# Kernel optimization log

Hardware: AMD Instinct MI355X
Metric: run time of the kernel (lower is better)

## Reference

```python
import jax, jax.numpy as jnp
import numpy as np

TEMPERATURE = 0.1

def setup_inputs() -> dict:
    key = jax.random.key(0)
    ks = jax.random.split(key, 6)
    B, K, D, H, N = 256, 32, 128, 256, 16
    z = jax.random.normal(ks[0], (B, K, D), dtype=jnp.float32)
    # edge MLP params: Linear(2D->H), GELU, Linear(H->D)
    W1 = jax.random.normal(ks[1], (2 * D, H), dtype=jnp.float32) * (1.0 / np.sqrt(2 * D))
    b1 = jnp.zeros((H,), dtype=jnp.float32)
    W2 = jax.random.normal(ks[2], (H, D), dtype=jnp.float32) * (1.0 / np.sqrt(H))
    b2 = jnp.zeros((D,), dtype=jnp.float32)
    codebook = jax.random.normal(ks[3], (N, D), dtype=jnp.float32) * 0.02
    return {"z": z, "W1": W1, "b1": b1, "W2": W2, "b2": b2, "codebook": codebook}

def reference(z, W1, b1, W2, b2, codebook):
    # z: (B,K,D). Edge MLP on concat([z_i, z_j]) == split-weight GEMMs,
    # avoiding materializing the (B,K,K,2D) concat tensor.
    D = z.shape[-1]
    h_i = jnp.einsum('bkd,dh->bkh', z, W1[:D])   # contribution of z_i
    h_j = jnp.einsum('bkd,dh->bkh', z, W1[D:])   # contribution of z_j
    h = h_i[:, :, None, :] + h_j[:, None, :, :] + b1       # (B,K,K,H)
    h = jax.nn.gelu(h, approximate=False)                    # torch nn.GELU default = exact erf
    e_ij = jnp.einsum('bijh,hd->bijd', h, W2) + b2           # (B,K,K,D)
    logits = jnp.einsum('bijd,nd->bijn', e_ij, codebook) / TEMPERATURE  # (B,K,K,N)
    alpha_ij = jax.nn.softmax(logits, axis=-1)
    m_ij = jnp.einsum('bijn,nd->bijd', alpha_ij, codebook)   # (B,K,K,D)
    return (m_ij, alpha_ij, e_ij, logits)
```

## Files before the change

kernel.cpp:

```cpp
#include <hip/hip_runtime.h>
#include <hip/hip_bf16.h>
#include <math.h>

#define BB 256
#define KK 32
#define DD 128
#define HH 256
#define NN 16
#define O0 ((size_t)0)
#define O1 ((size_t)33554432)
#define O2 ((size_t)37748736)
#define O3 ((size_t)71303168)

typedef float f32x4 __attribute__((ext_vector_type(4)));
typedef short s16x8 __attribute__((ext_vector_type(8)));

static __device__ __forceinline__ short f2bf(float x) {
  __hip_bfloat16 h = __float2bfloat16(x);
  return *reinterpret_cast<short*>(&h);
}
static __device__ __forceinline__ float bf2f(short s) {
  __hip_bfloat16 h;
  *reinterpret_cast<short*>(&h) = s;
  return __bfloat162float(h);
}

__global__ __launch_bounds__(256) void hproj_kernel(
    const float* __restrict__ z, const float* __restrict__ W1,
    float* __restrict__ Hi, float* __restrict__ Hj) {
  __shared__ float sz[16][128];
  const int tid = threadIdx.x;
  const int row0 = blockIdx.x * 16;

#pragma unroll
  for (int s = 0; s < 8; ++s) {
    int idx = tid + s * 256;
    int r = idx >> 7, c = idx & 127;
    sz[r][c] = z[(size_t)(row0 + r) * 128 + c];
  }
  __syncthreads();

  const int rg = tid >> 6;
  const int cg = tid & 63;
  const float* wbase = (cg < 32) ? (W1 + cg * 8) : (W1 + 128 * 256 + (cg - 32) * 8);

  float4 acc[4][2];
#pragma unroll
  for (int r = 0; r < 4; ++r) {
    acc[r][0] = make_float4(0.f, 0.f, 0.f, 0.f);
    acc[r][1] = make_float4(0.f, 0.f, 0.f, 0.f);
  }

  for (int d = 0; d < 128; ++d) {
    float4 w0 = *(const float4*)(wbase + (size_t)d * 256);
    float4 w1 = *(const float4*)(wbase + (size_t)d * 256 + 4);
#pragma unroll
    for (int r = 0; r < 4; ++r) {
      float a = sz[rg * 4 + r][d];
      acc[r][0].x += a * w0.x; acc[r][0].y += a * w0.y;
      acc[r][0].z += a * w0.z; acc[r][0].w += a * w0.w;
      acc[r][1].x += a * w1.x; acc[r][1].y += a * w1.y;
      acc[r][1].z += a * w1.z; acc[r][1].w += a * w1.w;
    }
  }

  float* obase = (cg < 32) ? (Hi + (size_t)(row0)*256 + cg * 8)
                           : (Hj + (size_t)(row0)*256 + (cg - 32) * 8);
#pragma unroll
  for (int r = 0; r < 4; ++r) {
    *(float4*)(obase + (size_t)(rg * 4 + r) * 256) = acc[r][0];
    *(float4*)(obase + (size_t)(rg * 4 + r) * 256 + 4) = acc[r][1];
  }
}

__global__ __launch_bounds__(256) void wprep_kernel(
    const float* __restrict__ W2, const float* __restrict__ cb,
    short* __restrict__ Wh, short* __restrict__ Wl,
    short* __restrict__ cbh, short* __restrict__ cbl) {
  int idx = blockIdx.x * 256 + threadIdx.x;
  int c = idx & 127, k = idx >> 7;
  float w = W2[(size_t)k * 128 + c];
  short hb = f2bf(w);
  short lb = f2bf(w - bf2f(hb));
  Wh[(size_t)c * 256 + k] = hb;
  Wl[(size_t)c * 256 + k] = lb;
  if (idx < 2048) {
    float v = cb[idx];
    short h = f2bf(v);
    cbh[idx] = h;
    cbl[idx] = f2bf(v - bf2f(h));
  }
}

__global__ __launch_bounds__(256, 3) void pair_kernel(
    const float* __restrict__ Hi, const float* __restrict__ Hj,
    const float* __restrict__ b1, const short* __restrict__ Wh,
    const short* __restrict__ Wl, const float* __restrict__ b2,
    const float* __restrict__ cb, const short* __restrict__ cbh,
    const short* __restrict__ cbl, float* __restrict__ out) {
  __shared__ short sAh[32 * 256];
  __shared__ union {
    short Al[32 * 256];
    struct { short Eh[32 * 128]; short El[32 * 128]; } e;
  } u;
  __shared__ float sCB[16 * 132];
  __shared__ float sAlp[32][16];

  const int tid = threadIdx.x;
  const int blk = blockIdx.x;
  const int b = blk >> 5;

#pragma unroll
  for (int s = 0; s < 8; ++s) {
    int idx = tid + s * 256;
    sCB[(idx >> 7) * 132 + (idx & 127)] = cb[idx];
  }

  {
    const int k0 = (tid & 127) * 2;
    const int pb = (tid >> 7) * 16;
    const float2 hiv = *(const float2*)(Hi + (size_t)blk * 256 + k0);
    const float2 b1v = *(const float2*)(b1 + k0);
    const float hx = hiv.x + b1v.x;
    const float hy = hiv.y + b1v.y;
    const float* hjp = Hj + ((size_t)b * KK + pb) * 256 + k0;
    unsigned* aH = (unsigned*)sAh;
    unsigned* aL = (unsigned*)u.Al;
    const int cw = tid & 127;
#pragma unroll 4
    for (int p = 0; p < 16; ++p) {
      const int row = pb + p;
      float2 hj = *(const float2*)(hjp + (size_t)p * 256);
      float x0 = hx + hj.x;
      float x1 = hy + hj.y;
      float g0 = 0.5f * x0 * (1.0f + erff(x0 * 0.70710678118654752f));
      float g1 = 0.5f * x1 * (1.0f + erff(x1 * 0.70710678118654752f));
      short h0 = f2bf(g0), h1 = f2bf(g1);
      short l0 = f2bf(g0 - bf2f(h0)), l1 = f2bf(g1 - bf2f(h1));
      const int wi = row * 128 + ((cw ^ ((row & 7) << 2)));
      aH[wi] = (unsigned)(unsigned short)h0 | ((unsigned)(unsigned short)h1 << 16);
      aL[wi] = (unsigned)(unsigned short)l0 | ((unsigned)(unsigned short)l1 << 16);
    }
  }
  __syncthreads();

  const int lane = tid & 63;
  const int wv = tid >> 6;
  const int nb = wv * 32;
  const int l4 = lane >> 4;
  const int l15 = lane & 15;

  f32x4 acc[2][2];
#pragma unroll
  for (int mt = 0; mt < 2; ++mt)
#pragma unroll
    for (int nt = 0; nt < 2; ++nt)
      acc[mt][nt] = (f32x4){0.f, 0.f, 0.f, 0.f};

  const int sw = (l15 & 7) << 4;
  const char* pAh = (const char*)sAh;
  const char* pAl = (const char*)u.Al;
  const size_t gB0 = (size_t)(nb + l15) * 256 + l4 * 8;

#pragma unroll
  for (int ks = 0; ks < 8; ++ks) {
    const int cbyte = ks * 64 + l4 * 16;
    const int o0 = l15 * 512 + (cbyte ^ sw);
    const int o1 = (16 + l15) * 512 + (cbyte ^ sw);
    s16x8 ah0 = *(const s16x8*)(pAh + o0);
    s16x8 ah1 = *(const s16x8*)(pAh + o1);
    s16x8 al0 = *(const s16x8*)(pAl + o0);
    s16x8 al1 = *(const s16x8*)(pAl + o1);
    const size_t g0 = gB0 + ks * 32;
    const size_t g1 = g0 + 16 * 256;
    s16x8 bh0 = *(const s16x8*)(Wh + g0);
    s16x8 bh1 = *(const s16x8*)(Wh + g1);
    s16x8 bl0 = *(const s16x8*)(Wl + g0);
    s16x8 bl1 = *(const s16x8*)(Wl + g1);

    acc[0][0] = __builtin_amdgcn_mfma_f32_16x16x32_bf16(ah0, bh0, acc[0][0], 0, 0, 0);
    acc[0][0] = __builtin_amdgcn_mfma_f32_16x16x32_bf16(al0, bh0, acc[0][0], 0, 0, 0);
    acc[0][0] = __builtin_amdgcn_mfma_f32_16x16x32_bf16(ah0, bl0, acc[0][0], 0, 0, 0);
    acc[0][1] = __builtin_amdgcn_mfma_f32_16x16x32_bf16(ah0, bh1, acc[0][1], 0, 0, 0);
    acc[0][1] = __builtin_amdgcn_mfma_f32_16x16x32_bf16(al0, bh1, acc[0][1], 0, 0, 0);
    acc[0][1] = __builtin_amdgcn_mfma_f32_16x16x32_bf16(ah0, bl1, acc[0][1], 0, 0, 0);
    acc[1][0] = __builtin_amdgcn_mfma_f32_16x16x32_bf16(ah1, bh0, acc[1][0], 0, 0, 0);
    acc[1][0] = __builtin_amdgcn_mfma_f32_16x16x32_bf16(al1, bh0, acc[1][0], 0, 0, 0);
    acc[1][0] = __builtin_amdgcn_mfma_f32_16x16x32_bf16(ah1, bl0, acc[1][0], 0, 0, 0);
    acc[1][1] = __builtin_amdgcn_mfma_f32_16x16x32_bf16(ah1, bh1, acc[1][1], 0, 0, 0);
    acc[1][1] = __builtin_amdgcn_mfma_f32_16x16x32_bf16(al1, bh1, acc[1][1], 0, 0, 0);
    acc[1][1] = __builtin_amdgcn_mfma_f32_16x16x32_bf16(ah1, bl1, acc[1][1], 0, 0, 0);
  }

  __syncthreads();

  {
    const float b2v0 = b2[nb + l15];
    const float b2v1 = b2[nb + 16 + l15];
    float* eg = out + O2 + (size_t)blk * (KK * DD);
    char* pEh = (char*)u.e.Eh;
    char* pEl = (char*)u.e.El;
#pragma unroll
    for (int mt = 0; mt < 2; ++mt) {
#pragma unroll
      for (int r = 0; r < 4; ++r) {
        const int row = mt * 16 + l4 * 4 + r;
        const int rsw = (row & 7) << 4;
        const float e0 = acc[mt][0][r] + b2v0;
        const float e1 = acc[mt][1][r] + b2v1;
        eg[row * 128 + nb + l15] = e0;
        eg[row * 128 + nb + 16 + l15] = e1;
        short h0 = f2bf(e0), h1 = f2bf(e1);
        short lo0 = f2bf(e0 - bf2f(h0)), lo1 = f2bf(e1 - bf2f(h1));
        const int i0 = row * 256 + (((nb + l15) * 2) ^ rsw);
        const int i1 = row * 256 + (((nb + 16 + l15) * 2) ^ rsw);
        *(short*)(pEh + i0) = h0;
        *(short*)(pEh + i1) = h1;
        *(short*)(pEl + i0) = lo0;
        *(short*)(pEl + i1) = lo1;
      }
    }
  }
  __syncthreads();

  if (wv < 2) {
    const int mrow = wv * 16;
    f32x4 lacc = (f32x4){0.f, 0.f, 0.f, 0.f};
    const char* pEh = (const char*)u.e.Eh;
    const char* pEl = (const char*)u.e.El;
    const int rowa = mrow + l15;
    const int rsw = (rowa & 7) << 4;
#pragma unroll
    for (int ks = 0; ks < 4; ++ks) {
      const int cbyte = ks * 64 + l4 * 16;
      const int o = rowa * 256 + (cbyte ^ rsw);
      s16x8 eh = *(const s16x8*)(pEh + o);
      s16x8 el = *(const s16x8*)(pEl + o);
      const size_t g = (size_t)l15 * 128 + ks * 32 + l4 * 8;
      s16x8 ch = *(const s16x8*)(cbh + g);
      s16x8 cl = *(const s16x8*)(cbl + g);
      lacc = __builtin_amdgcn_mfma_f32_16x16x32_bf16(eh, ch, lacc, 0, 0, 0);
      lacc = __builtin_amdgcn_mfma_f32_16x16x32_bf16(el, ch, lacc, 0, 0, 0);
      lacc = __builtin_amdgcn_mfma_f32_16x16x32_bf16(eh, cl, lacc, 0, 0, 0);
    }
    float* lg_out = out + O3 + (size_t)blk * (KK * NN);
    float* ag_out = out + O1 + (size_t)blk * (KK * NN);
#pragma unroll
    for (int r = 0; r < 4; ++r) {
      const int row = mrow + l4 * 4 + r;
      float lg = lacc[r] * 10.0f;
      float mx = lg;
#pragma unroll
      for (int m = 1; m < 16; m <<= 1) mx = fmaxf(mx, __shfl_xor(mx, m));
      float p = __expf(lg - mx);
      float s = p;
#pragma unroll
      for (int m = 1; m < 16; m <<= 1) s += __shfl_xor(s, m);
      float a = p / s;
      lg_out[row * 16 + l15] = lg;
      ag_out[row * 16 + l15] = a;
      sAlp[row][l15] = a;
    }
  }
  __syncthreads();

  {
    const int pg = tid >> 5;
    const int cg = tid & 31;
    float4 mac0 = make_float4(0.f, 0.f, 0.f, 0.f);
    float4 mac1 = mac0, mac2 = mac0, mac3 = mac0;
#pragma unroll
    for (int n4 = 0; n4 < 4; ++n4) {
      float4 q0 = *(const float4*)&sAlp[pg * 4 + 0][n4 * 4];
      float4 q1 = *(const float4*)&sAlp[pg * 4 + 1][n4 * 4];
      float4 q2 = *(const float4*)&sAlp[pg * 4 + 2][n4 * 4];
      float4 q3 = *(const float4*)&sAlp[pg * 4 + 3][n4 * 4];
#pragma unroll
      for (int nn = 0; nn < 4; ++nn) {
        const int n = n4 * 4 + nn;
        float4 cv = *(const float4*)&sCB[n * 132 + cg * 4];
        float a0 = (nn == 0) ? q0.x : (nn == 1) ? q0.y : (nn == 2) ? q0.z : q0.w;
        float a1 = (nn == 0) ? q1.x : (nn == 1) ? q1.y : (nn == 2) ? q1.z : q1.w;
        float a2 = (nn == 0) ? q2.x : (nn == 1) ? q2.y : (nn == 2) ? q2.z : q2.w;
        float a3 = (nn == 0) ? q3.x : (nn == 1) ? q3.y : (nn == 2) ? q3.z : q3.w;
        mac0.x += a0 * cv.x; mac0.y += a0 * cv.y; mac0.z += a0 * cv.z; mac0.w += a0 * cv.w;
        mac1.x += a1 * cv.x; mac1.y += a1 * cv.y; mac1.z += a1 * cv.z; mac1.w += a1 * cv.w;
        mac2.x += a2 * cv.x; mac2.y += a2 * cv.y; mac2.z += a2 * cv.z; mac2.w += a2 * cv.w;
        mac3.x += a3 * cv.x; mac3.y += a3 * cv.y; mac3.z += a3 * cv.z; mac3.w += a3 * cv.w;
      }
    }
    float* mg = out + O0 + (size_t)blk * (KK * DD);
    *(float4*)(mg + (size_t)(pg * 4 + 0) * 128 + cg * 4) = mac0;
    *(float4*)(mg + (size_t)(pg * 4 + 1) * 128 + cg * 4) = mac1;
    *(float4*)(mg + (size_t)(pg * 4 + 2) * 128 + cg * 4) = mac2;
    *(float4*)(mg + (size_t)(pg * 4 + 3) * 128 + cg * 4) = mac3;
  }
}

extern "C" void kernel_launch(void* const* d_in, const int* in_sizes, int n_in,
                              void* d_out, int out_size, void* d_ws, size_t ws_size,
                              hipStream_t stream) {
  const float* z  = (const float*)d_in[0];
  const float* W1 = (const float*)d_in[1];
  const float* b1 = (const float*)d_in[2];
  const float* W2 = (const float*)d_in[3];
  const float* b2 = (const float*)d_in[4];
  const float* cb = (const float*)d_in[5];
  float* out = (float*)d_out;

  float* Hi = (float*)d_ws;
  float* Hj = Hi + (size_t)8192 * 256;
  short* Wh = (short*)(Hj + (size_t)8192 * 256);
  short* Wl = Wh + (size_t)128 * 256;
  short* cbh = Wl + (size_t)128 * 256;
  short* cbl = cbh + (size_t)2048;

  hproj_kernel<<<512, 256, 0, stream>>>(z, W1, Hi, Hj);
  wprep_kernel<<<128, 256, 0, stream>>>(W2, cb, Wh, Wl, cbh, cbl);
  pair_kernel<<<BB * KK, 256, 0, stream>>>(Hi, Hj, b1, Wh, Wl, b2, cb, cbh, cbl, out);
}
```

Measured before the change: 240.7 us.

## Move H projection to bf16 MFMA, use polynomial erf GELU, drop codebook LDS

The scalar fp32 H projection is replaced by a bf16 MFMA kernel. z is rounded to a single bf16 and W1 is split into high and low bf16 parts, all in a merged prep kernel, and Hi/Hj are written as one concatenated buffer. In the pair kernel, erff is replaced by an Abramowitz-Stegun polynomial with a fast reciprocal and exp. The shared-memory codebook copy is dropped in favour of direct global loads, which frees LDS so occupancy can rise from 3 to 4 blocks. Rounding z to one bf16 and the approximate erf reduce accuracy.

New measurement: 209.3 us. 1.15x faster.

```diff
diff --git a/kernel.cpp b/kernel.cpp
--- a/kernel.cpp
+++ b/kernel.cpp
@@ -25,65 +25,43 @@
   return __bfloat162float(h);
 }
 
-__global__ __launch_bounds__(256) void hproj_kernel(
+static __device__ __forceinline__ float gelu_exact(float x) {
+  float ax = fabsf(x) * 0.70710678118654752f;
+  float t = __builtin_amdgcn_rcpf(fmaf(0.3275911f, ax, 1.0f));
+  float p = fmaf(1.061405429f, t, -1.453152027f);
+  p = fmaf(p, t, 1.421413741f);
+  p = fmaf(p, t, -0.284496736f);
+  p = fmaf(p, t, 0.254829592f);
+  p *= t;
+  float e = __expf(-ax * ax);
+  float er = fmaf(-p, e, 1.0f);
+  er = copysignf(er, x);
+  return 0.5f * x * (1.0f + er);
+}
+
+__global__ __launch_bounds__(256) void prep_kernel(
     const float* __restrict__ z, const float* __restrict__ W1,
-    float* __restrict__ Hi, float* __restrict__ Hj) {
-  __shared__ float sz[16][128];
-  const int tid = threadIdx.x;
-  const int row0 = blockIdx.x * 16;
-
-#pragma unroll
-  for (int s = 0; s < 8; ++s) {
-    int idx = tid + s * 256;
-    int r = idx >> 7, c = idx & 127;
-    sz[r][c] = z[(size_t)(row0 + r) * 128 + c];
-  }
-  __syncthreads();
-
-  const int rg = tid >> 6;
-  const int cg = tid & 63;
-  const float* wbase = (cg < 32) ? (W1 + cg * 8) : (W1 + 128 * 256 + (cg - 32) * 8);
-
-  float4 acc[4][2];
-#pragma unroll
-  for (int r = 0; r < 4; ++r) {
-    acc[r][0] = make_float4(0.f, 0.f, 0.f, 0.f);
-    acc[r][1] = make_float4(0.f, 0.f, 0.f, 0.f);
-  }
-
-  for (int d = 0; d < 128; ++d) {
-    float4 w0 = *(const float4*)(wbase + (size_t)d * 256);
-    float4 w1 = *(const float4*)(wbase + (size_t)d * 256 + 4);
-#pragma unroll
-    for (int r = 0; r < 4; ++r) {
-      float a = sz[rg * 4 + r][d];
-      acc[r][0].x += a * w0.x; acc[r][0].y += a * w0.y;
-      acc[r][0].z += a * w0.z; acc[r][0].w += a * w0.w;
-      acc[r][1].x += a * w1.x; acc[r][1].y += a * w1.y;
-      acc[r][1].z += a * w1.z; acc[r][1].w += a * w1.w;
-    }
-  }
-
-  float* obase = (cg < 32) ? (Hi + (size_t)(row0)*256 + cg * 8)
-                           : (Hj + (size_t)(row0)*256 + (cg - 32) * 8);
-#pragma unroll
-  for (int r = 0; r < 4; ++r) {
-    *(float4*)(obase + (size_t)(rg * 4 + r) * 256) = acc[r][0];
-    *(float4*)(obase + (size_t)(rg * 4 + r) * 256 + 4) = acc[r][1];
-  }
-}
-
-__global__ __launch_bounds__(256) void wprep_kernel(
     const float* __restrict__ W2, const float* __restrict__ cb,
+    short* __restrict__ zb, short* __restrict__ W1th, short* __restrict__ W1tl,
     short* __restrict__ Wh, short* __restrict__ Wl,
     short* __restrict__ cbh, short* __restrict__ cbl) {
-  int idx = blockIdx.x * 256 + threadIdx.x;
-  int c = idx & 127, k = idx >> 7;
-  float w = W2[(size_t)k * 128 + c];
-  short hb = f2bf(w);
-  short lb = f2bf(w - bf2f(hb));
-  Wh[(size_t)c * 256 + k] = hb;
-  Wl[(size_t)c * 256 + k] = lb;
+  const int idx = blockIdx.x * 256 + threadIdx.x;
+  zb[idx] = f2bf(z[idx]);
+  if (idx < 512 * 128) {
+    int c = idx >> 7, k = idx & 127;
+    float w = (c < 256) ? W1[(size_t)k * 256 + c]
+                        : W1[(size_t)(128 + k) * 256 + (c - 256)];
+    short h = f2bf(w);
+    W1th[idx] = h;
+    W1tl[idx] = f2bf(w - bf2f(h));
+  }
+  if (idx < 128 * 256) {
+    int c = idx >> 8, k = idx & 255;
+    float w = W2[(size_t)k * 128 + c];
+    short h = f2bf(w);
+    Wh[idx] = h;
+    Wl[idx] = f2bf(w - bf2f(h));
+  }
   if (idx < 2048) {
     float v = cb[idx];
     short h = f2bf(v);
@@ -92,49 +70,86 @@
   }
 }
 
-__global__ __launch_bounds__(256, 3) void pair_kernel(
-    const float* __restrict__ Hi, const float* __restrict__ Hj,
-    const float* __restrict__ b1, const short* __restrict__ Wh,
-    const short* __restrict__ Wl, const float* __restrict__ b2,
-    const float* __restrict__ cb, const short* __restrict__ cbh,
-    const short* __restrict__ cbl, float* __restrict__ out) {
+__global__ __launch_bounds__(256) void hproj_mfma(
+    const short* __restrict__ zb, const short* __restrict__ W1th,
+    const short* __restrict__ W1tl, float* __restrict__ H) {
+  const int tid = threadIdx.x;
+  const int lane = tid & 63;
+  const int wv = tid >> 6;
+  const int l4 = lane >> 4, l15 = lane & 15;
+  const int row0 = blockIdx.x * 32;
+  const int col0 = blockIdx.y * 128 + wv * 32;
+
+  f32x4 acc[2][2];
+#pragma unroll
+  for (int mt = 0; mt < 2; ++mt)
+#pragma unroll
+    for (int nt = 0; nt < 2; ++nt)
+      acc[mt][nt] = (f32x4){0.f, 0.f, 0.f, 0.f};
+
+#pragma unroll
+  for (int ks = 0; ks < 4; ++ks) {
+    const int kof = ks * 32 + l4 * 8;
+    s16x8 a0 = *(const s16x8*)(zb + (size_t)(row0 + l15) * 128 + kof);
+    s16x8 a1 = *(const s16x8*)(zb + (size_t)(row0 + 16 + l15) * 128 + kof);
+    s16x8 bh0 = *(const s16x8*)(W1th + (size_t)(col0 + l15) * 128 + kof);
+    s16x8 bh1 = *(const s16x8*)(W1th + (size_t)(col0 + 16 + l15) * 128 + kof);
+    s16x8 bl0 = *(const s16x8*)(W1tl + (size_t)(col0 + l15) * 128 + kof);
+    s16x8 bl1 = *(const s16x8*)(W1tl + (size_t)(col0 + 16 + l15) * 128 + kof);
+    acc[0][0] = __builtin_amdgcn_mfma_f32_16x16x32_bf16(a0, bh0, acc[0][0], 0, 0, 0);
+    acc[0][0] = __builtin_amdgcn_mfma_f32_16x16x32_bf16(a0, bl0, acc[0][0], 0, 0, 0);
+    acc[0][1] = __builtin_amdgcn_mfma_f32_16x16x32_bf16(a0, bh1, acc[0][1], 0, 0, 0);
+    acc[0][1] = __builtin_amdgcn_mfma_f32_16x16x32_bf16(a0, bl1, acc[0][1], 0, 0, 0);
+    acc[1][0] = __builtin_amdgcn_mfma_f32_16x16x32_bf16(a1, bh0, acc[1][0], 0, 0, 0);
+    acc[1][0] = __builtin_amdgcn_mfma_f32_16x16x32_bf16(a1, bl0, acc[1][0], 0, 0, 0);
+    acc[1][1] = __builtin_amdgcn_mfma_f32_16x16x32_bf16(a1, bh1, acc[1][1], 0, 0, 0);
+    acc[1][1] = __builtin_amdgcn_mfma_f32_16x16x32_bf16(a1, bl1, acc[1][1], 0, 0, 0);
+  }
+
+#pragma unroll
+  for (int mt = 0; mt < 2; ++mt)
+#pragma unroll
+    for (int nt = 0; nt < 2; ++nt)
+#pragma unroll
+      for (int r = 0; r < 4; ++r)
+        H[(size_t)(row0 + mt * 16 + l4 * 4 + r) * 512 + col0 + nt * 16 + l15] =
+            acc[mt][nt][r];
+}
+
+__global__ __launch_bounds__(256, 4) void pair_kernel(
+    const float* __restrict__ Hcat, const float* __restrict__ b1,
+    const short* __restrict__ Wh, const short* __restrict__ Wl,
+    const float* __restrict__ b2, const float* __restrict__ cb,
+    const short* __restrict__ cbh, const short* __restrict__ cbl,
+    float* __restrict__ out) {
   __shared__ short sAh[32 * 256];
   __shared__ union {
     short Al[32 * 256];
     struct { short Eh[32 * 128]; short El[32 * 128]; } e;
   } u;
-  __shared__ float sCB[16 * 132];
   __shared__ float sAlp[32][16];
 
   const int tid = threadIdx.x;
   const int blk = blockIdx.x;
   const int b = blk >> 5;
 
-#pragma unroll
-  for (int s = 0; s < 8; ++s) {
-    int idx = tid + s * 256;
-    sCB[(idx >> 7) * 132 + (idx & 127)] = cb[idx];
-  }
-
   {
     const int k0 = (tid & 127) * 2;
     const int pb = (tid >> 7) * 16;
-    const float2 hiv = *(const float2*)(Hi + (size_t)blk * 256 + k0);
+    const float2 hiv = *(const float2*)(Hcat + (size_t)blk * 512 + k0);
     const float2 b1v = *(const float2*)(b1 + k0);
     const float hx = hiv.x + b1v.x;
     const float hy = hiv.y + b1v.y;
-    const float* hjp = Hj + ((size_t)b * KK + pb) * 256 + k0;
+    const float* hjp = Hcat + ((size_t)b * KK + pb) * 512 + 256 + k0;
     unsigned* aH = (unsigned*)sAh;
     unsigned* aL = (unsigned*)u.Al;
     const int cw = tid & 127;
 #pragma unroll 4
     for (int p = 0; p < 16; ++p) {
       const int row = pb + p;
-      float2 hj = *(const float2*)(hjp + (size_t)p * 256);
-      float x0 = hx + hj.x;
-      float x1 = hy + hj.y;
-      float g0 = 0.5f * x0 * (1.0f + erff(x0 * 0.70710678118654752f));
-      float g1 = 0.5f * x1 * (1.0f + erff(x1 * 0.70710678118654752f));
+      float2 hj = *(const float2*)(hjp + (size_t)p * 512);
+      float g0 = gelu_exact(hx + hj.x);
+      float g1 = gelu_exact(hy + hj.y);
       short h0 = f2bf(g0), h1 = f2bf(g1);
       short l0 = f2bf(g0 - bf2f(h0)), l1 = f2bf(g1 - bf2f(h1));
       const int wi = row * 128 + ((cw ^ ((row & 7) << 2)));
@@ -267,27 +282,20 @@
   {
     const int pg = tid >> 5;
     const int cg = tid & 31;
+    const float4* cb4 = (const float4*)cb;
     float4 mac0 = make_float4(0.f, 0.f, 0.f, 0.f);
     float4 mac1 = mac0, mac2 = mac0, mac3 = mac0;
 #pragma unroll
-    for (int n4 = 0; n4 < 4; ++n4) {
-      float4 q0 = *(const float4*)&sAlp[pg * 4 + 0][n4 * 4];
-      float4 q1 = *(const float4*)&sAlp[pg * 4 + 1][n4 * 4];
-      float4 q2 = *(const float4*)&sAlp[pg * 4 + 2][n4 * 4];
-      float4 q3 = *(const float4*)&sAlp[pg * 4 + 3][n4 * 4];
-#pragma unroll
-      for (int nn = 0; nn < 4; ++nn) {
-        const int n = n4 * 4 + nn;
-        float4 cv = *(const float4*)&sCB[n * 132 + cg * 4];
-        float a0 = (nn == 0) ? q0.x : (nn == 1) ? q0.y : (nn == 2) ? q0.z : q0.w;
-        float a1 = (nn == 0) ? q1.x : (nn == 1) ? q1.y : (nn == 2) ? q1.z : q1.w;
-        float a2 = (nn == 0) ? q2.x : (nn == 1) ? q2.y : (nn == 2) ? q2.z : q2.w;
-        float a3 = (nn == 0) ? q3.x : (nn == 1) ? q3.y : (nn == 2) ? q3.z : q3.w;
-        mac0.x += a0 * cv.x; mac0.y += a0 * cv.y; mac0.z += a0 * cv.z; mac0.w += a0 * cv.w;
-        mac1.x += a1 * cv.x; mac1.y += a1 * cv.y; mac1.z += a1 * cv.z; mac1.w += a1 * cv.w;
-        mac2.x += a2 * cv.x; mac2.y += a2 * cv.y; mac2.z += a2 * cv.z; mac2.w += a2 * cv.w;
-        mac3.x += a3 * cv.x; mac3.y += a3 * cv.y; mac3.z += a3 * cv.z; mac3.w += a3 * cv.w;
-      }
+    for (int n = 0; n < 16; ++n) {
+      float4 cv = cb4[n * 32 + cg];
+      float a0 = sAlp[pg * 4 + 0][n];
+      float a1 = sAlp[pg * 4 + 1][n];
+      float a2 = sAlp[pg * 4 + 2][n];
+      float a3 = sAlp[pg * 4 + 3][n];
+      mac0.x += a0 * cv.x; mac0.y += a0 * cv.y; mac0.z += a0 * cv.z; mac0.w += a0 * cv.w;
+      mac1.x += a1 * cv.x; mac1.y += a1 * cv.y; mac1.z += a1 * cv.z; mac1.w += a1 * cv.w;
+      mac2.x += a2 * cv.x; mac2.y += a2 * cv.y; mac2.z += a2 * cv.z; mac2.w += a2 * cv.w;
+      mac3.x += a3 * cv.x; mac3.y += a3 * cv.y; mac3.z += a3 * cv.z; mac3.w += a3 * cv.w;
     }
     float* mg = out + O0 + (size_t)blk * (KK * DD);
     *(float4*)(mg + (size_t)(pg * 4 + 0) * 128 + cg * 4) = mac0;
@@ -308,14 +316,16 @@
   const float* cb = (const float*)d_in[5];
   float* out = (float*)d_out;
 
-  float* Hi = (float*)d_ws;
-  float* Hj = Hi + (size_t)8192 * 256;
-  short* Wh = (short*)(Hj + (size_t)8192 * 256);
-  short* Wl = Wh + (size_t)128 * 256;
-  short* cbh = Wl + (size_t)128 * 256;
-  short* cbl = cbh + (size_t)2048;
-
-  hproj_kernel<<<512, 256, 0, stream>>>(z, W1, Hi, Hj);
-  wprep_kernel<<<128, 256, 0, stream>>>(W2, cb, Wh, Wl, cbh, cbl);
-  pair_kernel<<<BB * KK, 256, 0, stream>>>(Hi, Hj, b1, Wh, Wl, b2, cb, cbh, cbl, out);
-}
+  float* Hcat = (float*)d_ws;
+  short* zb   = (short*)(Hcat + (size_t)8192 * 512);
+  short* W1th = zb + (size_t)1048576;
+  short* W1tl = W1th + (size_t)65536;
+  short* Wh   = W1tl + (size_t)65536;
+  short* Wl   = Wh + (size_t)32768;
+  short* cbh  = Wl + (size_t)32768;
+  short* cbl  = cbh + (size_t)2048;
+
+  prep_kernel<<<4096, 256, 0, stream>>>(z, W1, W2, cb, zb, W1th, W1tl, Wh, Wl, cbh, cbl);
+  hproj_mfma<<<dim3(256, 4), 256, 0, stream>>>(zb, W1th, W1tl, Hcat);
+  pair_kernel<<<BB * KK, 256, 0, stream>>>(Hcat, b1, Wh, Wl, b2, cb, cbh, cbl, out);
+}
```
